# Kernel tuning notes

Hardware: AMD Instinct MI355X
Metric: run time of the kernel (lower is better)

## Reference

```python
import jax, jax.numpy as jnp
import numpy as np

B, IN, OUT = 8192, 4096, 2048  # OUT must equal 32*64 per betta/gamma sizes


def setup_inputs() -> dict:
    key = jax.random.key(0)
    kx, kw = jax.random.split(key, 2)
    X = jax.random.normal(kx, (B, IN), dtype=jnp.float32)
    # xavier-uniform-like init for W
    limit = float(np.sqrt(6.0 / (IN + OUT)))
    W = jax.random.uniform(kw, (IN, OUT), minval=-limit, maxval=limit, dtype=jnp.float32)
    absmean = jnp.abs(W).mean(axis=0)
    alpha = jnp.abs(W).mean()          # scalar, >= 0
    betta = absmean[:32]               # (32,), >= 0
    gamma = absmean[32:96]             # (64,), >= 0
    return {"X": X, "W": W, "alpha": alpha, "betta": betta, "gamma": gamma}


def reference(X, W, alpha, betta, gamma):
    # module applies relu_ to alpha/betta/gamma data before the functional call
    alpha = jax.nn.relu(alpha)
    betta = jax.nn.relu(betta)
    gamma = jax.nn.relu(gamma)
    X_bin = jnp.sign(X)                # (B, IN)
    W_bin = jnp.sign(W)                # (IN, OUT)
    # scale[i*64+j] = alpha * betta[i] * gamma[j] -> (OUT,)
    scale = (alpha * jnp.outer(betta, gamma)).reshape(-1)
    return (X_bin @ W_bin) * scale     # (B, OUT)
```

## Files before the change

kernel.cpp:

```cpp
#include <hip/hip_runtime.h>


#define M_DIM 8192
#define K_DIM 4096
#define N_DIM 2048
#define NT    (K_DIM / 256)
#define TILE_BYTES 32768
#define PANEL_BYTES (NT * TILE_BYTES)

typedef int i32x4 __attribute__((ext_vector_type(4)));
typedef int i32x8 __attribute__((ext_vector_type(8)));
typedef float f32x16 __attribute__((ext_vector_type(16)));

__device__ __forceinline__ unsigned int nib4(float x) {
  unsigned int s = (__float_as_uint(x) >> 28) & 0x8u;
  return x == 0.0f ? 0u : (0x2u | s);
}

__device__ __forceinline__ unsigned int pack8(const float* f) {
  unsigned int p = 0;
#pragma unroll
  for (int j = 0; j < 8; ++j) p |= nib4(f[j]) << (4 * j);
  return p;
}

__device__ __forceinline__ void gload_lds16(const void* g, void* lds) {
  __builtin_amdgcn_global_load_lds(
      (const __attribute__((address_space(1))) unsigned int*)g,
      (__attribute__((address_space(3))) unsigned int*)lds, 16, 0, 0);
}

__device__ __forceinline__ i32x8 pad8(i32x4 v) {
  i32x8 r;
  r[0] = v[0]; r[1] = v[1]; r[2] = v[2]; r[3] = v[3];
  r[4] = 0; r[5] = 0; r[6] = 0; r[7] = 0;
  return r;
}

__global__ __launch_bounds__(256) void binX_kernel(
    const float* __restrict__ X, unsigned char* __restrict__ Xq) {
  const int t = threadIdx.x;
  const int s = t >> 5;
  const int r = t & 31;
  const int rg = blockIdx.x >> 4;
  const int kt = blockIdx.x & 15;
  const int row = rg * 32 + r;
  const int panel = row >> 8;

  const float* src = X + (size_t)row * K_DIM + kt * 256 + s * 32;
  float f[32];
#pragma unroll
  for (int i = 0; i < 8; ++i)
    *(float4*)&f[i * 4] = *(const float4*)&src[i * 4];
  uint4 gq;
  gq.x = pack8(f + 0);  gq.y = pack8(f + 8);
  gq.z = pack8(f + 16); gq.w = pack8(f + 24);
  unsigned char* dst = Xq + (size_t)panel * PANEL_BYTES + kt * TILE_BYTES +
                       ((size_t)s * 256 + (row & 255)) * 16;
  *(uint4*)dst = gq;
}

__global__ __launch_bounds__(256) void binW_kernel(
    const float* __restrict__ W, unsigned char* __restrict__ Wq) {
  __shared__ float tile[32][260];
  const int t = threadIdx.x;
  const int q = blockIdx.x >> 7;
  const int kt = (blockIdx.x >> 3) & 15;
  const int s = blockIdx.x & 7;

#pragma unroll
  for (int i = 0; i < 8; ++i) {
    int row = i * 4 + (t >> 6);
    int col4 = (t & 63) * 4;
    *(float4*)&tile[row][col4] =
        *(const float4*)&W[(size_t)(kt * 256 + s * 32 + row) * N_DIM + q * 256 + col4];
  }
  __syncthreads();
  float f[32];
#pragma unroll
  for (int k = 0; k < 32; ++k) f[k] = tile[k][t];
  uint4 gq;
  gq.x = pack8(f + 0);  gq.y = pack8(f + 8);
  gq.z = pack8(f + 16); gq.w = pack8(f + 24);
  unsigned char* dst = Wq + (size_t)q * PANEL_BYTES + kt * TILE_BYTES +
                       ((size_t)s * 256 + t) * 16;
  *(uint4*)dst = gq;
}

__device__ __forceinline__ void stage_tile(const unsigned char* __restrict__ src,
                                           unsigned char* lds, int t) {
#pragma unroll
  for (int p = 0; p < 4; ++p) {
    int c = p * 512 + t;
    gload_lds16(src + c * 16, lds + c * 16);
  }
}

__global__ __launch_bounds__(512, 2) void gemm_fp4_kernel(
    const unsigned char* __restrict__ Aq,
    const unsigned char* __restrict__ Bq,
    const float* __restrict__ alpha,
    const float* __restrict__ betta,
    const float* __restrict__ gamma,
    float* __restrict__ C) {
  __shared__ __align__(16) unsigned char smem[131072];

  const int t = threadIdx.x;
  const int lane = t & 63;
  const int l31 = lane & 31;
  const int lhi = lane >> 5;
  const int w = t >> 6;
  const int wr = w >> 2;
  const int wc = w & 3;

  const int bid = blockIdx.x;
  const int bn = bid & 7;
  const int bm = bid >> 3;
  const int row0 = bm * 256;
  const int col0 = bn * 256;

  const unsigned char* Abase = Aq + (size_t)bm * PANEL_BYTES;
  const unsigned char* Bbase = Bq + (size_t)bn * PANEL_BYTES;

  f32x16 acc[4][2];
#pragma unroll
  for (int fm = 0; fm < 4; ++fm)
#pragma unroll
    for (int fn = 0; fn < 2; ++fn)
#pragma unroll
      for (int r = 0; r < 16; ++r) acc[fm][fn][r] = 0.f;

  stage_tile(Abase, &smem[0], t);
  stage_tile(Bbase, &smem[32768], t);
  asm volatile("s_waitcnt vmcnt(0)" ::: "memory");
  __builtin_amdgcn_s_barrier();

  for (int kt = 0; kt < NT; ++kt) {
    const int cur = kt & 1;
    const unsigned char* pA = &smem[cur * 65536];
    const unsigned char* pB = pA + 32768;

#pragma unroll
    for (int kk = 0; kk < 4; ++kk) {
      const int g = kk * 2 + lhi;
      i32x4 a4[4], b4[2];
#pragma unroll
      for (int fm = 0; fm < 4; ++fm)
        a4[fm] = *(const i32x4*)&pA[(g * 256 + wr * 128 + fm * 32 + l31) * 16];
#pragma unroll
      for (int fn = 0; fn < 2; ++fn)
        b4[fn] = *(const i32x4*)&pB[(g * 256 + wc * 64 + fn * 32 + l31) * 16];

      if (kk == 0 && kt + 1 < NT)
        stage_tile(Abase + (kt + 1) * TILE_BYTES, &smem[(cur ^ 1) * 65536], t);
      if (kk == 1 && kt + 1 < NT)
        stage_tile(Bbase + (kt + 1) * TILE_BYTES, &smem[(cur ^ 1) * 65536 + 32768], t);

      __builtin_amdgcn_s_barrier();
      asm volatile("s_waitcnt lgkmcnt(0)" ::: "memory");
      __builtin_amdgcn_sched_barrier(0);
      __builtin_amdgcn_s_setprio(1);
#pragma unroll
      for (int fm = 0; fm < 4; ++fm) {
        i32x8 av = pad8(a4[fm]);
#pragma unroll
        for (int fn = 0; fn < 2; ++fn)
          acc[fm][fn] = __builtin_amdgcn_mfma_scale_f32_32x32x64_f8f6f4(
              av, pad8(b4[fn]), acc[fm][fn], 4, 4,
              0, 0x7F7F7F7F, 0, 0x7F7F7F7F);
      }
      __builtin_amdgcn_s_setprio(0);
    }
    asm volatile("s_waitcnt vmcnt(0)" ::: "memory");
    __builtin_amdgcn_s_barrier();
  }

  const float ra = fmaxf(alpha[0], 0.0f);
#pragma unroll
  for (int fn = 0; fn < 2; ++fn) {
    const int col = col0 + wc * 64 + fn * 32 + l31;
    const float sc = ra * fmaxf(betta[col >> 6], 0.0f) * fmaxf(gamma[col & 63], 0.0f);
#pragma unroll
    for (int fm = 0; fm < 4; ++fm) {
      const int rbase = row0 + wr * 128 + fm * 32 + 4 * lhi;
#pragma unroll
      for (int r = 0; r < 16; ++r) {
        const int row = rbase + (r & 3) + 8 * (r >> 2);
        C[(size_t)row * N_DIM + col] = acc[fm][fn][r] * sc;
      }
    }
  }
}

extern "C" void kernel_launch(void* const* d_in, const int* in_sizes, int n_in,
                              void* d_out, int out_size, void* d_ws, size_t ws_size,
                              hipStream_t stream) {
  const float* X = (const float*)d_in[0];
  const float* W = (const float*)d_in[1];
  const float* alpha = (const float*)d_in[2];
  const float* betta = (const float*)d_in[3];
  const float* gamma = (const float*)d_in[4];
  float* out = (float*)d_out;

  unsigned char* Xq = (unsigned char*)d_ws;
  unsigned char* Wq = Xq + (size_t)(M_DIM / 256) * PANEL_BYTES;

  binW_kernel<<<1024, 256, 0, stream>>>(W, Wq);
  binX_kernel<<<4096, 256, 0, stream>>>(X, Xq);
  gemm_fp4_kernel<<<(M_DIM / 256) * (N_DIM / 256), 512, 0, stream>>>(
      Xq, Wq, alpha, betta, gamma, out);
}
```

Before: 76.05 us.

## Double-buffer LDS fragment loads in fp4 GEMM and coalesce binX via LDS transpose

The GEMM inner loop now prefetches the next k-step's A/B fragments from LDS into a second register buffer while the MFMAs for the current step run, and drops the per-kk barrier. The first fragments of each new tile are loaded right after the tile-boundary barrier. binX now stages a 32x256 tile of X through shared memory with coalesced float4 loads before packing, instead of strided per-thread row reads. This adds register pressure from the doubled fragment buffers and relies on the remaining barriers to keep LDS reads ordered against the async global-to-LDS writes.

```diff
diff --git a/kernel.cpp b/kernel.cpp
--- a/kernel.cpp
+++ b/kernel.cpp
@@ -39,23 +39,27 @@
 
 __global__ __launch_bounds__(256) void binX_kernel(
     const float* __restrict__ X, unsigned char* __restrict__ Xq) {
+  __shared__ float tile[32][260];
   const int t = threadIdx.x;
+  const int rg = blockIdx.x >> 4;
+  const int kt = blockIdx.x & 15;
+  const int lrow = t >> 6;
+  const int col4 = (t & 63) * 4;
+#pragma unroll
+  for (int i = 0; i < 8; ++i)
+    *(float4*)&tile[i * 4 + lrow][col4] =
+        *(const float4*)&X[(size_t)(rg * 32 + i * 4 + lrow) * K_DIM + kt * 256 + col4];
+  __syncthreads();
   const int s = t >> 5;
   const int r = t & 31;
-  const int rg = blockIdx.x >> 4;
-  const int kt = blockIdx.x & 15;
-  const int row = rg * 32 + r;
-  const int panel = row >> 8;
-
-  const float* src = X + (size_t)row * K_DIM + kt * 256 + s * 32;
   float f[32];
 #pragma unroll
-  for (int i = 0; i < 8; ++i)
-    *(float4*)&f[i * 4] = *(const float4*)&src[i * 4];
+  for (int j = 0; j < 32; ++j) f[j] = tile[r][s * 32 + j];
   uint4 gq;
   gq.x = pack8(f + 0);  gq.y = pack8(f + 8);
   gq.z = pack8(f + 16); gq.w = pack8(f + 24);
-  unsigned char* dst = Xq + (size_t)panel * PANEL_BYTES + kt * TILE_BYTES +
+  const int row = rg * 32 + r;
+  unsigned char* dst = Xq + (size_t)(row >> 8) * PANEL_BYTES + kt * TILE_BYTES +
                        ((size_t)s * 256 + (row & 255)) * 16;
   *(uint4*)dst = gq;
 }
@@ -67,7 +71,6 @@
   const int q = blockIdx.x >> 7;
   const int kt = (blockIdx.x >> 3) & 15;
   const int s = blockIdx.x & 7;
-
 #pragma unroll
   for (int i = 0; i < 8; ++i) {
     int row = i * 4 + (t >> 6);
@@ -94,6 +97,18 @@
     int c = p * 512 + t;
     gload_lds16(src + c * 16, lds + c * 16);
   }
+}
+
+__device__ __forceinline__ void load_frags(i32x4* a4, i32x4* b4,
+                                           const unsigned char* pA,
+                                           const unsigned char* pB,
+                                           int g, int wr, int wc, int l31) {
+#pragma unroll
+  for (int fm = 0; fm < 4; ++fm)
+    a4[fm] = *(const i32x4*)&pA[(g * 256 + wr * 128 + fm * 32 + l31) * 16];
+#pragma unroll
+  for (int fn = 0; fn < 2; ++fn)
+    b4[fn] = *(const i32x4*)&pB[(g * 256 + wc * 64 + fn * 32 + l31) * 16];
 }
 
 __global__ __launch_bounds__(512, 2) void gemm_fp4_kernel(
@@ -135,6 +150,9 @@
   asm volatile("s_waitcnt vmcnt(0)" ::: "memory");
   __builtin_amdgcn_s_barrier();
 
+  i32x4 a4[2][4], b4[2][2];
+  load_frags(a4[0], b4[0], &smem[0], &smem[32768], lhi, wr, wc, l31);
+
   for (int kt = 0; kt < NT; ++kt) {
     const int cur = kt & 1;
     const unsigned char* pA = &smem[cur * 65536];
@@ -142,37 +160,34 @@
 
 #pragma unroll
     for (int kk = 0; kk < 4; ++kk) {
-      const int g = kk * 2 + lhi;
-      i32x4 a4[4], b4[2];
-#pragma unroll
-      for (int fm = 0; fm < 4; ++fm)
-        a4[fm] = *(const i32x4*)&pA[(g * 256 + wr * 128 + fm * 32 + l31) * 16];
-#pragma unroll
-      for (int fn = 0; fn < 2; ++fn)
-        b4[fn] = *(const i32x4*)&pB[(g * 256 + wc * 64 + fn * 32 + l31) * 16];
-
+      const int pb = kk & 1, pn = pb ^ 1;
+      asm volatile("s_waitcnt lgkmcnt(0)" ::: "memory");
+      __builtin_amdgcn_sched_barrier(0);
       if (kk == 0 && kt + 1 < NT)
         stage_tile(Abase + (kt + 1) * TILE_BYTES, &smem[(cur ^ 1) * 65536], t);
       if (kk == 1 && kt + 1 < NT)
         stage_tile(Bbase + (kt + 1) * TILE_BYTES, &smem[(cur ^ 1) * 65536 + 32768], t);
-
-      __builtin_amdgcn_s_barrier();
-      asm volatile("s_waitcnt lgkmcnt(0)" ::: "memory");
+      if (kk < 3)
+        load_frags(a4[pn], b4[pn], pA, pB, (kk + 1) * 2 + lhi, wr, wc, l31);
       __builtin_amdgcn_sched_barrier(0);
       __builtin_amdgcn_s_setprio(1);
 #pragma unroll
       for (int fm = 0; fm < 4; ++fm) {
-        i32x8 av = pad8(a4[fm]);
+        i32x8 av = pad8(a4[pb][fm]);
 #pragma unroll
         for (int fn = 0; fn < 2; ++fn)
           acc[fm][fn] = __builtin_amdgcn_mfma_scale_f32_32x32x64_f8f6f4(
-              av, pad8(b4[fn]), acc[fm][fn], 4, 4,
+              av, pad8(b4[pb][fn]), acc[fm][fn], 4, 4,
               0, 0x7F7F7F7F, 0, 0x7F7F7F7F);
       }
       __builtin_amdgcn_s_setprio(0);
     }
     asm volatile("s_waitcnt vmcnt(0)" ::: "memory");
     __builtin_amdgcn_s_barrier();
+    if (kt + 1 < NT) {
+      const unsigned char* nA = &smem[((kt + 1) & 1) * 65536];
+      load_frags(a4[0], b4[0], nA, nA + 32768, lhi, wr, wc, l31);
+    }
   }
 
   const float ra = fmaxf(alpha[0], 0.0f);
```

After: 75.34 us. About the same (-0.9%).
